# Optimization experiments

Measured on AMD Instinct MI355X. Metric: run time of the kernel, lower is better.

Reference implementation:

```python
import jax, jax.numpy as jnp
import numpy as np

N_QUBITS = 6
N_LAYERS = 3
FEATURE_DIM = 512
ENC_HIDDEN = max(32, N_QUBITS * 4)  # 32
HEAD_HIDDEN = 128
G, T = 54, 24
DIM = 2 ** N_QUBITS  # 64


def _ry_batched(angles):
    # angles: [B] -> batched RY matrices [B, 2, 2] (complex64)
    c = jnp.cos(angles * 0.5)
    s = jnp.sin(angles * 0.5)
    U = jnp.stack([jnp.stack([c, -s], -1), jnp.stack([s, c], -1)], -2)
    return U.astype(jnp.complex64)


def _rot(phi, theta, omega):
    # PennyLane Rot = RZ(omega) RY(theta) RZ(phi); returns [2, 2] complex64
    c = jnp.cos(theta * 0.5).astype(jnp.complex64)
    s = jnp.sin(theta * 0.5).astype(jnp.complex64)
    ep = jnp.exp(-0.5j * (phi + omega).astype(jnp.complex64))  # e^{-i(phi+omega)/2}
    em = jnp.exp(-0.5j * (phi - omega).astype(jnp.complex64))  # e^{-i(phi-omega)/2}
    u00 = ep * c
    u01 = -jnp.conj(em) * s
    u10 = em * s
    u11 = jnp.conj(ep) * c
    return jnp.stack([jnp.stack([u00, u01]), jnp.stack([u10, u11])])


def _apply_1q_batched(state, U, q):
    # state: [B, 2^n]; U: [B, 2, 2] (per-sample gate, e.g. data-encoding RY)
    B = state.shape[0]
    st = state.reshape(B, 2 ** q, 2, -1)
    st = jnp.einsum('bij,bljr->blir', U, st)
    return st.reshape(B, -1)


def _apply_1q(state, U, q):
    # state: [B, 2^n]; U: [2, 2] shared across batch (trainable Rot)
    B = state.shape[0]
    st = state.reshape(B, 2 ** q, 2, -1)
    st = jnp.einsum('ij,bljr->blir', U, st)
    return st.reshape(B, -1)


def _apply_cnot(state, c, t):
    # state: [B, 2^n]; flip target axis where control bit == 1
    B = state.shape[0]
    st = state.reshape((B,) + (2,) * N_QUBITS)
    ax_c, ax_t = 1 + c, 1 + t
    s0 = jnp.take(st, 0, axis=ax_c)
    s1 = jnp.take(st, 1, axis=ax_c)
    s1 = jnp.flip(s1, axis=ax_t if ax_t < ax_c else ax_t - 1)
    st = jnp.stack([s0, s1], axis=ax_c)
    return st.reshape(B, -1)


def _expvals_z(state):
    # <Z_q> for every qubit: [B, n]
    B = state.shape[0]
    probs = (state.real ** 2 + state.imag ** 2).reshape((B,) + (2,) * N_QUBITS)
    outs = []
    for q in range(N_QUBITS):
        axes = tuple(i for i in range(1, N_QUBITS + 1) if i != q + 1)
        p = probs.sum(axes)  # [B, 2]
        outs.append(p[:, 0] - p[:, 1])
    return jnp.stack(outs, -1)


def _circuit(angles, q_weights):
    # angles: [B, n_qubits] float32; q_weights: [L, n, 3]
    B = angles.shape[0]
    state = jnp.zeros((B, DIM), jnp.complex64).at[:, 0].set(1.0)
    for layer in range(N_LAYERS):
        # data_reuploading=True -> re-encode every layer
        for q in range(N_QUBITS):
            state = _apply_1q_batched(state, _ry_batched(angles[:, q]), q)
        for q in range(N_QUBITS):
            w = q_weights[layer, q]
            state = _apply_1q(state, _rot(w[0], w[1], w[2]), q)
        for q in range(0, N_QUBITS - 1, 2):
            state = _apply_cnot(state, q, q + 1)
        for q in range(1, N_QUBITS - 1, 2):
            state = _apply_cnot(state, q, q + 1)
        state = _apply_cnot(state, N_QUBITS - 1, 0)  # n_qubits > 2
    return _expvals_z(state)


def setup_inputs() -> dict:
    key = jax.random.key(0)
    ks = jax.random.split(key, 10)
    B = 32768
    return {
        'x': jax.random.normal(ks[0], (B, FEATURE_DIM), jnp.float32),
        'enc_w1': 0.05 * jax.random.normal(ks[1], (FEATURE_DIM, ENC_HIDDEN), jnp.float32),
        'enc_b1': jnp.zeros((ENC_HIDDEN,), jnp.float32),
        'enc_w2': 0.05 * jax.random.normal(ks[2], (ENC_HIDDEN, N_QUBITS), jnp.float32),
        'enc_b2': jnp.zeros((N_QUBITS,), jnp.float32),
        'q_weights': 0.01 * jax.random.normal(ks[3], (N_LAYERS, N_QUBITS, 3), jnp.float32),
        'head_w1': 0.1 * jax.random.normal(ks[4], (N_QUBITS, HEAD_HIDDEN), jnp.float32),
        'head_b1': jnp.zeros((HEAD_HIDDEN,), jnp.float32),
        'head_w2': 0.05 * jax.random.normal(ks[5], (HEAD_HIDDEN, G * T), jnp.float32),
        'head_b2': jnp.zeros((G * T,), jnp.float32),
    }


def reference(x, enc_w1, enc_b1, enc_w2, enc_b2, q_weights,
              head_w1, head_b1, head_w2, head_b2):
    # classical encoder -> angles [B, n_qubits]
    h = jnp.tanh(x @ enc_w1 + enc_b1)
    angles = h @ enc_w2 + enc_b2
    # batched state-vector PQC simulation
    z = _circuit(angles, q_weights).astype(jnp.float32)  # [B, n_qubits]
    # classical head (dropout is identity in eval)
    g = jax.nn.relu(z @ head_w1 + head_b1)
    logits = g @ head_w2 + head_b2
    return logits.reshape(-1, G, T)
```

## Files before the change

### kernel.cpp

```cpp
#include <hip/hip_runtime.h>

typedef __bf16 bf16x8 __attribute__((ext_vector_type(8)));
typedef float floatx4 __attribute__((ext_vector_type(4)));
typedef unsigned short ushort8 __attribute__((ext_vector_type(8)));

__device__ __forceinline__ unsigned short f2bf(float f) {
    unsigned u = __float_as_uint(f);
    u += 0x7fffu + ((u >> 16) & 1u);
    return (unsigned short)(u >> 16);
}

__global__ void prep_kernel(const float* __restrict__ w2, const float* __restrict__ qw,
                            unsigned short* __restrict__ w2t, float* __restrict__ umat) {
    int t = blockIdx.x * 256 + threadIdx.x;
    if (t < 18) {
        float phi = qw[t * 3], theta = qw[t * 3 + 1], omega = qw[t * 3 + 2];
        float c = cosf(0.5f * theta), s = sinf(0.5f * theta);
        float po = 0.5f * (phi + omega), pm = 0.5f * (phi - omega);
        float epr = cosf(po), epi = -sinf(po);
        float emr = cosf(pm), emi = -sinf(pm);
        float* u = umat + t * 8;
        u[0] = epr * c;  u[1] = epi * c;
        u[2] = -emr * s; u[3] = emi * s;
        u[4] = emr * s;  u[5] = emi * s;
        u[6] = epr * c;  u[7] = -epi * c;
    }
    if (t < 128 * 1296) {
        int nn = t >> 7, kk = t & 127;
        w2t[t] = f2bf(w2[kk * 1296 + nn]);
    }
}

__global__ __launch_bounds__(256) void enc_kernel(
    const float* __restrict__ x, const float* __restrict__ w1,
    const float* __restrict__ b1, const float* __restrict__ w2,
    const float* __restrict__ b2, float* __restrict__ angles) {
    __shared__ float part[4][64][33];
    __shared__ float hsh[64][33];
    int lane = threadIdx.x & 63;
    int wave = threadIdx.x >> 6;
    int swave = __builtin_amdgcn_readfirstlane(wave);
    size_t row = (size_t)blockIdx.x * 64 + lane;
    const float4* x4 = (const float4*)(x + row * 512 + swave * 128);
    const float* wbase = w1 + swave * 128 * 32;

    float acc[32];
#pragma unroll
    for (int j = 0; j < 32; ++j) acc[j] = 0.f;
#pragma unroll 2
    for (int k4 = 0; k4 < 32; ++k4) {
        float4 xv = x4[k4];
        const float* wr = wbase + k4 * 128;
#pragma unroll
        for (int j = 0; j < 32; ++j) acc[j] += xv.x * wr[j];
#pragma unroll
        for (int j = 0; j < 32; ++j) acc[j] += xv.y * wr[32 + j];
#pragma unroll
        for (int j = 0; j < 32; ++j) acc[j] += xv.z * wr[64 + j];
#pragma unroll
        for (int j = 0; j < 32; ++j) acc[j] += xv.w * wr[96 + j];
    }
#pragma unroll
    for (int j = 0; j < 32; ++j) part[wave][lane][j] = acc[j];
    __syncthreads();

    int rl = threadIdx.x & 63;
    int jg = (threadIdx.x >> 6) * 8;
#pragma unroll
    for (int jj = 0; jj < 8; ++jj) {
        int j = jg + jj;
        float v = part[0][rl][j] + part[1][rl][j] + part[2][rl][j] + part[3][rl][j] + b1[j];
        hsh[rl][j] = tanhf(v);
    }
    __syncthreads();

    if (threadIdx.x < 64) {
        float h[32];
#pragma unroll
        for (int j = 0; j < 32; ++j) h[j] = hsh[threadIdx.x][j];
#pragma unroll
        for (int q = 0; q < 6; ++q) {
            float a = b2[q];
#pragma unroll
            for (int j = 0; j < 32; ++j) a += h[j] * w2[j * 6 + q];
            angles[((size_t)blockIdx.x * 64 + threadIdx.x) * 6 + q] = a;
        }
    }
}

template <int ST>
__device__ __forceinline__ void apply_g(float* sr, float* si,
    float m00r, float m00i, float m01r, float m01i,
    float m10r, float m10i, float m11r, float m11i) {
#pragma unroll
    for (int i = 0; i < 64; ++i) {
        if ((i & ST) == 0) {
            int i1 = i + ST;
            float r0 = sr[i], u0 = si[i], r1 = sr[i1], u1 = si[i1];
            sr[i]  = m00r * r0 - m00i * u0 + m01r * r1 - m01i * u1;
            si[i]  = m00r * u0 + m00i * r0 + m01r * u1 + m01i * r1;
            sr[i1] = m10r * r0 - m10i * u0 + m11r * r1 - m11i * u1;
            si[i1] = m10r * u0 + m10i * r0 + m11r * u1 + m11i * r1;
        }
    }
}

template <int CB, int TB>
__device__ __forceinline__ void cnot_g(float* sr, float* si) {
#pragma unroll
    for (int i = 0; i < 64; ++i) {
        if ((i & CB) && !(i & TB)) {
            int i1 = i + TB;
            float tr = sr[i]; sr[i] = sr[i1]; sr[i1] = tr;
            float ti = si[i]; si[i] = si[i1]; si[i1] = ti;
        }
    }
}

__global__ __launch_bounds__(64) void quantum_kernel(
    const float* __restrict__ angles, const float* __restrict__ umat,
    const float* __restrict__ hw1, const float* __restrict__ hb1,
    unsigned short* __restrict__ g) {
    int s = blockIdx.x * 64 + threadIdx.x;
    float ca[6], sa[6];
#pragma unroll
    for (int q = 0; q < 6; ++q) {
        float a = 0.5f * angles[(size_t)s * 6 + q];
        ca[q] = cosf(a);
        sa[q] = sinf(a);
    }
    float sr[64], si[64];
#pragma unroll
    for (int i = 0; i < 64; ++i) { sr[i] = 0.f; si[i] = 0.f; }
    sr[0] = 1.f;

#pragma clang loop unroll(disable)
    for (int layer = 0; layer < 3; ++layer) {
        const float* ub = umat + layer * 48;
#define DOQ(Q, ST) {                                                      \
        const float* u = ub + (Q) * 8;                                    \
        float c = ca[Q], ss = sa[Q];                                      \
        float m00r = u[0] * c + u[2] * ss, m00i = u[1] * c + u[3] * ss;   \
        float m01r = u[2] * c - u[0] * ss, m01i = u[3] * c - u[1] * ss;   \
        float m10r = u[4] * c + u[6] * ss, m10i = u[5] * c + u[7] * ss;   \
        float m11r = u[6] * c - u[4] * ss, m11i = u[7] * c - u[5] * ss;   \
        apply_g<ST>(sr, si, m00r, m00i, m01r, m01i, m10r, m10i, m11r, m11i); }
        DOQ(0, 32) DOQ(1, 16) DOQ(2, 8) DOQ(3, 4) DOQ(4, 2) DOQ(5, 1)
#undef DOQ
        cnot_g<32, 16>(sr, si);
        cnot_g<8, 4>(sr, si);
        cnot_g<2, 1>(sr, si);
        cnot_g<16, 8>(sr, si);
        cnot_g<4, 2>(sr, si);
        cnot_g<1, 32>(sr, si);
    }

    float z[6] = {0.f, 0.f, 0.f, 0.f, 0.f, 0.f};
#pragma unroll
    for (int i = 0; i < 64; ++i) {
        float p = sr[i] * sr[i] + si[i] * si[i];
        z[0] += (i & 32) ? -p : p;
        z[1] += (i & 16) ? -p : p;
        z[2] += (i & 8)  ? -p : p;
        z[3] += (i & 4)  ? -p : p;
        z[4] += (i & 2)  ? -p : p;
        z[5] += (i & 1)  ? -p : p;
    }

    unsigned short* gp = g + (size_t)s * 128;
#pragma unroll 2
    for (int j0 = 0; j0 < 128; j0 += 8) {
        ushort8 pk;
#pragma unroll
        for (int jj = 0; jj < 8; ++jj) {
            int j = j0 + jj;
            float a = hb1[j];
#pragma unroll
            for (int q = 0; q < 6; ++q) a += z[q] * hw1[q * 128 + j];
            a = fmaxf(a, 0.f);
            pk[jj] = f2bf(a);
        }
        *(ushort8*)(gp + j0) = pk;
    }
}

__global__ __launch_bounds__(256) void head_gemm(
    const unsigned short* __restrict__ g, const unsigned short* __restrict__ w2t,
    const float* __restrict__ b2, float* __restrict__ out) {
    int lane = threadIdx.x & 63;
    int task = blockIdx.x * 4 + (threadIdx.x >> 6);
    int m = task / 81;
    int n = task - m * 81;
    int row0 = m * 64, col0 = n * 16;
    int l15 = lane & 15, quad = lane >> 4;

    const unsigned short* bp = w2t + (size_t)(col0 + l15) * 128 + quad * 8;
    const unsigned short* ap = g + (size_t)(row0 + l15) * 128 + quad * 8;

    floatx4 acc[4];
#pragma unroll
    for (int t = 0; t < 4; ++t) acc[t] = (floatx4)0.f;

#pragma unroll
    for (int ks = 0; ks < 4; ++ks) {
        bf16x8 bf = *(const bf16x8*)(bp + ks * 32);
#pragma unroll
        for (int sub = 0; sub < 4; ++sub) {
            bf16x8 af = *(const bf16x8*)(ap + sub * 16 * 128 + ks * 32);
            acc[sub] = __builtin_amdgcn_mfma_f32_16x16x32_bf16(af, bf, acc[sub], 0, 0, 0);
        }
    }

    float bias = b2[col0 + l15];
#pragma unroll
    for (int sub = 0; sub < 4; ++sub) {
#pragma unroll
        for (int i = 0; i < 4; ++i) {
            int r = row0 + sub * 16 + quad * 4 + i;
            out[(size_t)r * 1296 + col0 + l15] = acc[sub][i] + bias;
        }
    }
}

extern "C" void kernel_launch(void* const* d_in, const int* in_sizes, int n_in,
                              void* d_out, int out_size, void* d_ws, size_t ws_size,
                              hipStream_t stream) {
    const float* x   = (const float*)d_in[0];
    const float* ew1 = (const float*)d_in[1];
    const float* eb1 = (const float*)d_in[2];
    const float* ew2 = (const float*)d_in[3];
    const float* eb2 = (const float*)d_in[4];
    const float* qw  = (const float*)d_in[5];
    const float* hw1 = (const float*)d_in[6];
    const float* hb1 = (const float*)d_in[7];
    const float* hw2 = (const float*)d_in[8];
    const float* hb2 = (const float*)d_in[9];
    float* out = (float*)d_out;

    char* ws = (char*)d_ws;
    unsigned short* g   = (unsigned short*)(ws);
    unsigned short* w2t = (unsigned short*)(ws + 8388608);
    float* angles       = (float*)(ws + 8720384);
    float* umat         = (float*)(ws + 9506816);

    prep_kernel<<<dim3(648), dim3(256), 0, stream>>>(hw2, qw, w2t, umat);
    enc_kernel<<<dim3(512), dim3(256), 0, stream>>>(x, ew1, eb1, ew2, eb2, angles);
    quantum_kernel<<<dim3(512), dim3(64), 0, stream>>>(angles, umat, hw1, hb1, g);
    head_gemm<<<dim3(10368), dim3(256), 0, stream>>>(g, w2t, hb2, out);
}
```

Baseline: 384.3 us.

## Widen head GEMM tiles, vectorize output stores, and restructure prep and encoder loops

The head GEMM now gives each wave a 64x48 output tile instead of 64x16. Operands are swapped so every lane writes four consecutive output columns as a single vectorized nontemporal store. Each A/B fragment load is reused across more MFMAs, and the launch uses a third as many blocks. The weight transpose in prep now packs eight bf16 values per thread with 16-byte stores, and the encoder inner loop switches to float2 loads with explicit fmaf and unrolling disabled. The larger accumulator set raises register pressure, and the new tiling cuts the number of waves available to hide latency.

```diff
diff --git a/kernel.cpp b/kernel.cpp
--- a/kernel.cpp
+++ b/kernel.cpp
@@ -10,8 +10,9 @@
     return (unsigned short)(u >> 16);
 }
 
-__global__ void prep_kernel(const float* __restrict__ w2, const float* __restrict__ qw,
-                            unsigned short* __restrict__ w2t, float* __restrict__ umat) {
+__global__ __launch_bounds__(256) void prep_kernel(
+    const float* __restrict__ w2, const float* __restrict__ qw,
+    unsigned short* __restrict__ w2t, float* __restrict__ umat) {
     int t = blockIdx.x * 256 + threadIdx.x;
     if (t < 18) {
         float phi = qw[t * 3], theta = qw[t * 3 + 1], omega = qw[t * 3 + 2];
@@ -25,9 +26,13 @@
         u[4] = emr * s;  u[5] = emi * s;
         u[6] = epr * c;  u[7] = -epi * c;
     }
-    if (t < 128 * 1296) {
-        int nn = t >> 7, kk = t & 127;
-        w2t[t] = f2bf(w2[kk * 1296 + nn]);
+    int nn = t >> 4;
+    int kc = (t & 15) * 8;
+    if (nn < 1296) {
+        ushort8 pk;
+#pragma unroll
+        for (int j = 0; j < 8; ++j) pk[j] = f2bf(w2[(size_t)(kc + j) * 1296 + nn]);
+        *(ushort8*)(w2t + (size_t)nn * 128 + kc) = pk;
     }
 }
 
@@ -41,24 +46,21 @@
     int wave = threadIdx.x >> 6;
     int swave = __builtin_amdgcn_readfirstlane(wave);
     size_t row = (size_t)blockIdx.x * 64 + lane;
-    const float4* x4 = (const float4*)(x + row * 512 + swave * 128);
-    const float* wbase = w1 + swave * 128 * 32;
+    const float2* x2 = (const float2*)(x + row * 512 + swave * 128);
+    const float* wseg = w1 + swave * 128 * 32;
 
     float acc[32];
 #pragma unroll
     for (int j = 0; j < 32; ++j) acc[j] = 0.f;
-#pragma unroll 2
-    for (int k4 = 0; k4 < 32; ++k4) {
-        float4 xv = x4[k4];
-        const float* wr = wbase + k4 * 128;
-#pragma unroll
-        for (int j = 0; j < 32; ++j) acc[j] += xv.x * wr[j];
-#pragma unroll
-        for (int j = 0; j < 32; ++j) acc[j] += xv.y * wr[32 + j];
-#pragma unroll
-        for (int j = 0; j < 32; ++j) acc[j] += xv.z * wr[64 + j];
-#pragma unroll
-        for (int j = 0; j < 32; ++j) acc[j] += xv.w * wr[96 + j];
+
+#pragma clang loop unroll(disable)
+    for (int k2 = 0; k2 < 64; ++k2) {
+        float2 xv = x2[k2];
+        const float* wr = wseg + k2 * 64;
+#pragma unroll
+        for (int j = 0; j < 32; ++j) acc[j] = fmaf(wr[j], xv.x, acc[j]);
+#pragma unroll
+        for (int j = 0; j < 32; ++j) acc[j] = fmaf(wr[32 + j], xv.y, acc[j]);
     }
 #pragma unroll
     for (int j = 0; j < 32; ++j) part[wave][lane][j] = acc[j];
@@ -82,7 +84,7 @@
         for (int q = 0; q < 6; ++q) {
             float a = b2[q];
 #pragma unroll
-            for (int j = 0; j < 32; ++j) a += h[j] * w2[j * 6 + q];
+            for (int j = 0; j < 32; ++j) a = fmaf(h[j], w2[j * 6 + q], a);
             angles[((size_t)blockIdx.x * 64 + threadIdx.x) * 6 + q] = a;
         }
     }
@@ -176,7 +178,7 @@
             int j = j0 + jj;
             float a = hb1[j];
 #pragma unroll
-            for (int q = 0; q < 6; ++q) a += z[q] * hw1[q * 128 + j];
+            for (int q = 0; q < 6; ++q) a = fmaf(z[q], hw1[q * 128 + j], a);
             a = fmaxf(a, 0.f);
             pk[jj] = f2bf(a);
         }
@@ -189,35 +191,41 @@
     const float* __restrict__ b2, float* __restrict__ out) {
     int lane = threadIdx.x & 63;
     int task = blockIdx.x * 4 + (threadIdx.x >> 6);
-    int m = task / 81;
-    int n = task - m * 81;
-    int row0 = m * 64, col0 = n * 16;
+    int m = task / 27;
+    int n = task - m * 27;
+    int row0 = m * 64, col0 = n * 48;
     int l15 = lane & 15, quad = lane >> 4;
 
-    const unsigned short* bp = w2t + (size_t)(col0 + l15) * 128 + quad * 8;
-    const unsigned short* ap = g + (size_t)(row0 + l15) * 128 + quad * 8;
-
-    floatx4 acc[4];
-#pragma unroll
-    for (int t = 0; t < 4; ++t) acc[t] = (floatx4)0.f;
+    const unsigned short* ap = w2t + (size_t)(col0 + l15) * 128 + quad * 8;
+    const unsigned short* bp = g + (size_t)(row0 + l15) * 128 + quad * 8;
+
+    floatx4 acc[12];
+#pragma unroll
+    for (int i = 0; i < 12; ++i) acc[i] = (floatx4)0.f;
 
 #pragma unroll
     for (int ks = 0; ks < 4; ++ks) {
-        bf16x8 bf = *(const bf16x8*)(bp + ks * 32);
+        bf16x8 af[3], bf[4];
+#pragma unroll
+        for (int t = 0; t < 3; ++t) af[t] = *(const bf16x8*)(ap + (size_t)t * 16 * 128 + ks * 32);
+#pragma unroll
+        for (int sub = 0; sub < 4; ++sub) bf[sub] = *(const bf16x8*)(bp + (size_t)sub * 16 * 128 + ks * 32);
+#pragma unroll
+        for (int t = 0; t < 3; ++t)
+#pragma unroll
+            for (int sub = 0; sub < 4; ++sub)
+                acc[t * 4 + sub] = __builtin_amdgcn_mfma_f32_16x16x32_bf16(af[t], bf[sub], acc[t * 4 + sub], 0, 0, 0);
+    }
+
+#pragma unroll
+    for (int t = 0; t < 3; ++t) {
+        const float* bb = b2 + col0 + t * 16 + quad * 4;
+        floatx4 bias = { bb[0], bb[1], bb[2], bb[3] };
 #pragma unroll
         for (int sub = 0; sub < 4; ++sub) {
-            bf16x8 af = *(const bf16x8*)(ap + sub * 16 * 128 + ks * 32);
-            acc[sub] = __builtin_amdgcn_mfma_f32_16x16x32_bf16(af, bf, acc[sub], 0, 0, 0);
-        }
-    }
-
-    float bias = b2[col0 + l15];
-#pragma unroll
-    for (int sub = 0; sub < 4; ++sub) {
-#pragma unroll
-        for (int i = 0; i < 4; ++i) {
-            int r = row0 + sub * 16 + quad * 4 + i;
-            out[(size_t)r * 1296 + col0 + l15] = acc[sub][i] + bias;
+            floatx4 v = acc[t * 4 + sub] + bias;
+            floatx4* dst = (floatx4*)(out + (size_t)(row0 + sub * 16 + l15) * 1296 + col0 + t * 16 + quad * 4);
+            __builtin_nontemporal_store(v, dst);
         }
     }
 }
@@ -243,8 +251,8 @@
     float* angles       = (float*)(ws + 8720384);
     float* umat         = (float*)(ws + 9506816);
 
-    prep_kernel<<<dim3(648), dim3(256), 0, stream>>>(hw2, qw, w2t, umat);
+    prep_kernel<<<dim3(81), dim3(256), 0, stream>>>(hw2, qw, w2t, umat);
     enc_kernel<<<dim3(512), dim3(256), 0, stream>>>(x, ew1, eb1, ew2, eb2, angles);
     quantum_kernel<<<dim3(512), dim3(64), 0, stream>>>(angles, umat, hw1, hb1, g);
-    head_gemm<<<dim3(10368), dim3(256), 0, stream>>>(g, w2t, hb2, out);
-}
+    head_gemm<<<dim3(3456), dim3(256), 0, stream>>>(g, w2t, hb2, out);
+}
```

Result: faster. 318.9 us (-17.0%).
